# Optimization experiments

Measured on AMD Instinct MI355X. Metric: run time of the kernel, lower is better.

## Reference

```python
import jax, jax.numpy as jnp
from jax import lax
import numpy as np

D_MODEL, D_STATE, D_CONV, EXPAND = 192, 16, 3, 2
D_INNER = EXPAND * D_MODEL
B_, H_, W_ = 8, 128, 128
PAD = (D_CONV - 1) // 2
EPS = 1e-5


def setup_inputs() -> dict:
    key = jax.random.key(0)
    ks = jax.random.split(key, 8)
    s = 0.02
    return {
        "x": jax.random.normal(ks[0], (B_, D_MODEL, H_, W_), jnp.float32),
        "w_in": jax.random.normal(ks[1], (D_MODEL, 2 * D_INNER), jnp.float32) * s,
        "w_conv": jax.random.normal(ks[2], (D_INNER, 1, D_CONV, D_CONV), jnp.float32) * s,
        "b_conv": jnp.zeros((D_INNER,), jnp.float32),
        "w_x": jax.random.normal(ks[3], (D_INNER, 2 * D_STATE), jnp.float32) * s,
        "w_dt": jax.random.normal(ks[4], (D_STATE, D_INNER), jnp.float32) * s,
        "b_dt": jnp.zeros((D_INNER,), jnp.float32),
        "D_skip": jnp.ones((D_INNER,), jnp.float32),
        "w_out": jax.random.normal(ks[5], (D_INNER, D_MODEL), jnp.float32) * s,
        "gamma": jnp.ones((D_INNER,), jnp.float32),
        "beta": jnp.zeros((D_INNER,), jnp.float32),
    }


def _ss2d(x, w_in, w_conv, b_conv, w_x, w_dt, b_dt, D_skip, w_out, gamma, beta):
    B, C, H, W = x.shape
    L = H * W
    # NOTE: faithful to torch: x.reshape(B, H*W, C) on an NCHW tensor is a raw
    # row-major reinterpretation (same semantics as jnp.reshape), not a transpose.
    x_flat = x.reshape(B, L, C)
    x_proj = x_flat @ w_in                     # [B, L, 2*d_inner]
    x_inner, z = jnp.split(x_proj, 2, axis=-1)
    # depthwise conv over spatial dims
    xc = jnp.transpose(x_inner, (0, 2, 1)).reshape(B, D_INNER, H, W)
    xc = lax.conv_general_dilated(
        xc, w_conv, window_strides=(1, 1), padding=[(PAD, PAD), (PAD, PAD)],
        dimension_numbers=("NCHW", "OIHW", "NCHW"), feature_group_count=D_INNER,
    ) + b_conv[None, :, None, None]
    xc = jax.nn.silu(xc)
    xc = jnp.transpose(xc.reshape(B, D_INNER, L), (0, 2, 1))   # [B, L, d_inner]
    x_ssm = xc @ w_x                                            # [B, L, 2*d_state]
    B_ssm, C_ssm = jnp.split(x_ssm, 2, axis=-1)
    dt = jax.nn.softplus(B_ssm @ w_dt + b_dt)                   # [B, L, d_inner]
    # Original: deltaB = dt[...,None]*B_ssm[:,:,None,:]; einsum('blid,bld->bli', deltaB, C_ssm)
    # == dt * sum_d(B_ssm*C_ssm)  (deltaA is computed but never used -> dropped)
    bc = jnp.sum(B_ssm * C_ssm, axis=-1, keepdims=True)         # [B, L, 1]
    y = dt * bc + xc * D_skip                                   # [B, L, d_inner]
    y = y * jax.nn.silu(z)
    mu = jnp.mean(y, axis=-1, keepdims=True)
    var = jnp.mean(jnp.square(y - mu), axis=-1, keepdims=True)
    y = (y - mu) * lax.rsqrt(var + EPS) * gamma + beta
    out = y @ w_out                                             # [B, L, d_model]
    return jnp.transpose(out, (0, 2, 1)).reshape(B, C, H, W)


def reference(x, w_in, w_conv, b_conv, w_x, w_dt, b_dt, D_skip, w_out, gamma, beta):
    return _ss2d(x, w_in, w_conv, b_conv, w_x, w_dt, b_dt, D_skip, w_out, gamma, beta)
```

## Files before the change

### kernel.cpp

```cpp
#include <hip/hip_runtime.h>
#include <hip/hip_bf16.h>

typedef __bf16 bf16x8 __attribute__((ext_vector_type(8)));
typedef __bf16 bf16x4 __attribute__((ext_vector_type(4)));
typedef float  f32x4  __attribute__((ext_vector_type(4)));

__device__ __forceinline__ f32x4 mfma16(bf16x8 a, bf16x8 b, f32x4 c) {
    return __builtin_amdgcn_mfma_f32_16x16x32_bf16(a, b, c, 0, 0, 0);
}
__device__ __forceinline__ float silu_f(float v) { return v / (1.f + __expf(-v)); }
__device__ __forceinline__ float softplus_fast(float v) {
    float r = __logf(1.f + __expf(v));
    return v > 15.f ? v : r;
}

#define CC 192
#define DI 384
#define LL 16384
#define HH 128
#define WW 128

__global__ void k0_prep(const float* __restrict__ w_in, const float* __restrict__ w_x,
                        const float* __restrict__ w_dt, const float* __restrict__ w_out,
                        __bf16* __restrict__ wt_in, __bf16* __restrict__ wt_x,
                        __bf16* __restrict__ wt_dt, __bf16* __restrict__ wt_out) {
    int tid = blockIdx.x * blockDim.x + threadIdx.x;
    int nth = gridDim.x * blockDim.x;
    for (int i = tid; i < 768 * 192; i += nth) { int n = i / 192, k = i % 192; wt_in[i] = (__bf16)w_in[k * 768 + n]; }
    for (int i = tid; i < 32 * 384;  i += nth) { int n = i / 384, k = i % 384; wt_x[i]  = (__bf16)w_x[k * 32 + n]; }
    for (int i = tid; i < 384 * 16;  i += nth) { int ch = i / 16, k = i % 16;  wt_dt[i] = (__bf16)w_dt[k * 384 + ch]; }
    for (int i = tid; i < 192 * 384; i += nth) { int n = i / 384, k = i % 384; wt_out[i] = (__bf16)w_out[k * 192 + n]; }
}

__global__ __launch_bounds__(256, 4) void k1_proj(
        const float* __restrict__ x, const __bf16* __restrict__ wt_in,
        __bf16* __restrict__ xin, __bf16* __restrict__ zsb) {
    __shared__ __attribute__((aligned(16))) __bf16 wb[4 * 2 * 32 * 68];
    const int tid = threadIdx.x;
    const int lane = tid & 63, wv = tid >> 6;
    const int lq = lane & 15, quad = lane >> 4;
    const long mbase = (long)blockIdx.x * 128;
    __bf16* wbase = wb + wv * (2 * 32 * 68);

    bf16x8 af[2][6];
#pragma unroll
    for (int mt = 0; mt < 2; mt++) {
        const float* xr = x + (mbase + wv * 32 + mt * 16 + lq) * CC;
#pragma unroll
        for (int ks = 0; ks < 6; ks++) {
            float4 v0 = *(const float4*)(xr + ks * 32 + quad * 8);
            float4 v1 = *(const float4*)(xr + ks * 32 + quad * 8 + 4);
            bf16x8 t;
            t[0] = (__bf16)v0.x; t[1] = (__bf16)v0.y; t[2] = (__bf16)v0.z; t[3] = (__bf16)v0.w;
            t[4] = (__bf16)v1.x; t[5] = (__bf16)v1.y; t[6] = (__bf16)v1.z; t[7] = (__bf16)v1.w;
            af[mt][ks] = t;
        }
    }

    for (int nc = 0; nc < 12; nc++) {
        f32x4 A0[4], A1[4];
#pragma unroll
        for (int nt = 0; nt < 4; nt++) {
            A0[nt] = (f32x4){0.f, 0.f, 0.f, 0.f};
            A1[nt] = (f32x4){0.f, 0.f, 0.f, 0.f};
#pragma unroll
            for (int ks = 0; ks < 6; ks++) {
                bf16x8 bf = *(const bf16x8*)(wt_in + (long)(nc * 64 + nt * 16 + lq) * CC + ks * 32 + quad * 8);
                A0[nt] = mfma16(af[0][ks], bf, A0[nt]);
                A1[nt] = mfma16(af[1][ks], bf, A1[nt]);
            }
        }
        const bool isz = (nc >= 6);
        __bf16* bb = wbase + (nc & 1) * (32 * 68);
#pragma unroll
        for (int nt = 0; nt < 4; nt++) {
#pragma unroll
            for (int r = 0; r < 4; r++) {
                float v0 = A0[nt][r], v1 = A1[nt][r];
                if (isz) { v0 = silu_f(v0); v1 = silu_f(v1); }
                bb[(quad * 4 + r) * 68 + nt * 16 + lq] = (__bf16)v0;
                bb[(16 + quad * 4 + r) * 68 + nt * 16 + lq] = (__bf16)v1;
            }
        }
        __builtin_amdgcn_wave_barrier();
        __bf16* dst = isz ? zsb : xin;
        const int chb = (isz ? nc - 6 : nc) * 64;
#pragma unroll
        for (int k = 0; k < 4; k++) {
            int u = lane + k * 64;
            int row = u >> 3, c8 = u & 7;
            unsigned long long lo = *(const unsigned long long*)(&bb[row * 68 + c8 * 8]);
            unsigned long long hi = *(const unsigned long long*)(&bb[row * 68 + c8 * 8 + 4]);
            ulonglong2 val; val.x = lo; val.y = hi;
            *(ulonglong2*)(dst + (mbase + wv * 32 + row) * DI + chb + c8 * 8) = val;
        }
        __builtin_amdgcn_wave_barrier();
    }
}

__global__ __launch_bounds__(512, 4) void k3_ssm(
        const __bf16* __restrict__ xin, const __bf16* __restrict__ zsb,
        const __bf16* __restrict__ wtx, const __bf16* __restrict__ wtdt,
        const __bf16* __restrict__ wtout, const float* __restrict__ wconv,
        const float* __restrict__ bconv, const float* __restrict__ bdt,
        const float* __restrict__ dskip, const float* __restrict__ gamma,
        const float* __restrict__ beta, float* __restrict__ out) {
    __shared__ __attribute__((aligned(16))) float smem0[13056];
    __shared__ __attribute__((aligned(16))) __bf16 dts[64 * 200];
    __shared__ float bcarr[64];
    __bf16* xcb = (__bf16*)smem0;
    float* otile = smem0;

    const int tid = threadIdx.x;
    const int lane = tid & 63, wv = tid >> 6;
    const int lq = lane & 15, quad = lane >> 4;
    const int t0g = blockIdx.x * 64;

    const int te = tid >> 3, part = tid & 7;
    const long tok = t0g + te;

    bf16x8 zpre[6];
#pragma unroll
    for (int h = 0; h < 2; h++)
#pragma unroll
        for (int g = 0; g < 3; g++)
            zpre[h * 3 + g] = *(const bf16x8*)(zsb + tok * DI + h * 192 + part * 24 + g * 8);

    float* wcvs = (float*)dts;
    float* bcvs = wcvs + 9 * 384;
    for (int u = tid; u < 9 * 384; u += 512) { int ch = u / 9, tap = u % 9; wcvs[tap * 384 + ch] = wconv[u]; }
    for (int u = tid; u < 384; u += 512) bcvs[u] = bconv[u];
    __syncthreads();

    const int hblk = (t0g & (LL - 1)) >> 7;
    const int w0 = t0g & 127;
#pragma unroll
    for (int k = 0; k < 6; k++) {
        int u = tid + k * 512;
        int t = u / 48, c8 = u % 48;
        long tk = t0g + t;
        float acc[8];
        float4 b0 = *(const float4*)(bcvs + c8 * 8);
        float4 b1 = *(const float4*)(bcvs + c8 * 8 + 4);
        acc[0] = b0.x; acc[1] = b0.y; acc[2] = b0.z; acc[3] = b0.w;
        acc[4] = b1.x; acc[5] = b1.y; acc[6] = b1.z; acc[7] = b1.w;
#pragma unroll
        for (int dy = -1; dy <= 1; dy++) {
            int h2 = hblk + dy;
            if (h2 < 0 || h2 >= HH) continue;
#pragma unroll
            for (int dx = -1; dx <= 1; dx++) {
                int w2 = w0 + t + dx;
                if (w2 < 0 || w2 >= WW) continue;
                bf16x8 v = *(const bf16x8*)(xin + (tk + dy * WW + dx) * (long)DI + c8 * 8);
                const float* wp = &wcvs[((dy + 1) * 3 + (dx + 1)) * 384 + c8 * 8];
#pragma unroll
                for (int j = 0; j < 8; j++) acc[j] += (float)v[j] * wp[j];
            }
        }
        bf16x8 r;
#pragma unroll
        for (int j = 0; j < 8; j++) r[j] = (__bf16)silu_f(acc[j]);
        *(bf16x8*)(&xcb[t * 392 + c8 * 8]) = r;
    }
    __syncthreads();

    float* Bf = (float*)dts;
    float* Cf = Bf + 64 * 20;
    {
        const int wt = wv & 3, wsel = wv >> 2;
        f32x4 a4 = {0.f, 0.f, 0.f, 0.f};
#pragma unroll
        for (int ks = 0; ks < 12; ks++) {
            bf16x8 a = *(const bf16x8*)(&xcb[(wt * 16 + lq) * 392 + ks * 32 + quad * 8]);
            bf16x8 b = *(const bf16x8*)(wtx + (wsel * 16 + lq) * 384 + ks * 32 + quad * 8);
            a4 = mfma16(a, b, a4);
        }
        float* dstf = wsel ? Cf : Bf;
#pragma unroll
        for (int r = 0; r < 4; r++)
            dstf[(wt * 16 + quad * 4 + r) * 20 + lq] = a4[r];
    }
    __syncthreads();

    {
        int t = tid >> 3;
        int s0 = (tid & 7) * 2;
        float p = Bf[t * 20 + s0] * Cf[t * 20 + s0] + Bf[t * 20 + s0 + 1] * Cf[t * 20 + s0 + 1];
        p += __shfl_xor(p, 1, 64);
        p += __shfl_xor(p, 2, 64);
        p += __shfl_xor(p, 4, 64);
        if ((lane & 7) == 0) bcarr[t] = p;
    }
    bf16x8 zero8;
#pragma unroll
    for (int j = 0; j < 8; j++) zero8[j] = (__bf16)0.f;
    bf16x8 aA[4];
#pragma unroll
    for (int mt = 0; mt < 4; mt++) {
        if (quad < 2) {
            const float* bp = Bf + (mt * 16 + lq) * 20 + quad * 8;
            f32x4 lo = *(const f32x4*)(bp);
            f32x4 hi = *(const f32x4*)(bp + 4);
            bf16x8 t8;
            t8[0] = (__bf16)lo[0]; t8[1] = (__bf16)lo[1]; t8[2] = (__bf16)lo[2]; t8[3] = (__bf16)lo[3];
            t8[4] = (__bf16)hi[0]; t8[5] = (__bf16)hi[1]; t8[6] = (__bf16)hi[2]; t8[7] = (__bf16)hi[3];
            aA[mt] = t8;
        } else {
            aA[mt] = zero8;
        }
    }
    __syncthreads();

    float s1 = 0.f, s2 = 0.f;

#pragma unroll
    for (int h = 0; h < 2; h++) {
        f32x4 dacc[2][4];
        float bdtv[2];
#pragma unroll
        for (int j = 0; j < 2; j++) {
            const int tile = wv + 8 * j;
            if (tile < 12) {
                int chg = h * 192 + tile * 16 + lq;
                bf16x8 bf = (quad < 2) ? *(const bf16x8*)(wtdt + (long)chg * 16 + quad * 8) : zero8;
                bdtv[j] = bdt[chg];
#pragma unroll
                for (int mt = 0; mt < 4; mt++) {
                    f32x4 z4 = {0.f, 0.f, 0.f, 0.f};
                    dacc[j][mt] = mfma16(aA[mt], bf, z4);
                }
            }
        }
#pragma unroll
        for (int j = 0; j < 2; j++) {
            const int tile = wv + 8 * j;
            if (tile < 12) {
#pragma unroll
                for (int mt = 0; mt < 4; mt++)
#pragma unroll
                    for (int r = 0; r < 4; r++)
                        dts[(mt * 16 + quad * 4 + r) * 200 + tile * 16 + lq] =
                            (__bf16)(dacc[j][mt][r] + bdtv[j]);
            }
        }
        __syncthreads();

#pragma unroll
        for (int g = 0; g < 3; g++) {
            const int chl = part * 24 + g * 8;
            const int chg = h * 192 + chl;
            bf16x8 d8 = *(const bf16x8*)(&dts[te * 200 + chl]);
            bf16x8 xc8 = *(const bf16x8*)(&xcb[te * 392 + chg]);
            bf16x8 z8 = zpre[h * 3 + g];
            float4 d0 = *(const float4*)(dskip + chg);
            float4 d1 = *(const float4*)(dskip + chg + 4);
            float ds[8] = {d0.x, d0.y, d0.z, d0.w, d1.x, d1.y, d1.z, d1.w};
            const float bcv = bcarr[te];
#pragma unroll
            for (int j = 0; j < 8; j++) {
                float dtv = softplus_fast((float)d8[j]);
                float yv = (dtv * bcv + (float)xc8[j] * ds[j]) * (float)z8[j];
                s1 += yv; s2 += yv * yv;
                xc8[j] = (__bf16)yv;
            }
            *(bf16x8*)(&xcb[te * 392 + chg]) = xc8;
        }
        __syncthreads();
    }

    {
        s1 += __shfl_xor(s1, 1, 64); s2 += __shfl_xor(s2, 1, 64);
        s1 += __shfl_xor(s1, 2, 64); s2 += __shfl_xor(s2, 2, 64);
        s1 += __shfl_xor(s1, 4, 64); s2 += __shfl_xor(s2, 4, 64);
        float mu = s1 * (1.f / 384.f);
        float var = s2 * (1.f / 384.f) - mu * mu;
        float rstd = rsqrtf(var + 1e-5f);
#pragma unroll
        for (int gg = 0; gg < 6; gg++) {
            const int h2 = gg / 3, g3 = gg % 3;
            const int ch = h2 * 192 + part * 24 + g3 * 8;
            bf16x8 v = *(const bf16x8*)(&xcb[te * 392 + ch]);
            float4 g0 = *(const float4*)(gamma + ch);
            float4 g1 = *(const float4*)(gamma + ch + 4);
            float4 be0 = *(const float4*)(beta + ch);
            float4 be1 = *(const float4*)(beta + ch + 4);
            float gm[8] = {g0.x, g0.y, g0.z, g0.w, g1.x, g1.y, g1.z, g1.w};
            float bt[8] = {be0.x, be0.y, be0.z, be0.w, be1.x, be1.y, be1.z, be1.w};
#pragma unroll
            for (int j = 0; j < 8; j++) v[j] = (__bf16)(((float)v[j] - mu) * rstd * gm[j] + bt[j]);
            *(bf16x8*)(&xcb[te * 392 + ch]) = v;
        }
    }
    __syncthreads();

    {
        const int mh = wv >> 2, nb = (wv & 3) * 3;
        f32x4 acc[3][2];
#pragma unroll
        for (int j = 0; j < 3; j++)
#pragma unroll
            for (int m2 = 0; m2 < 2; m2++) acc[j][m2] = (f32x4){0.f, 0.f, 0.f, 0.f};
#pragma unroll
        for (int ks = 0; ks < 12; ks++) {
            bf16x8 bfr[3];
#pragma unroll
            for (int j = 0; j < 3; j++) {
                int c = (nb + j) * 16 + lq;
                bfr[j] = *(const bf16x8*)(wtout + (long)c * 384 + ks * 32 + quad * 8);
            }
#pragma unroll
            for (int m2 = 0; m2 < 2; m2++) {
                bf16x8 afr = *(const bf16x8*)(&xcb[((mh * 2 + m2) * 16 + lq) * 392 + ks * 32 + quad * 8]);
#pragma unroll
                for (int j = 0; j < 3; j++) acc[j][m2] = mfma16(afr, bfr[j], acc[j][m2]);
            }
        }
        __syncthreads();
#pragma unroll
        for (int j = 0; j < 3; j++) {
            int c = (nb + j) * 16 + lq;
#pragma unroll
            for (int m2 = 0; m2 < 2; m2++)
#pragma unroll
                for (int r = 0; r < 4; r++)
                    otile[c * 68 + (mh * 2 + m2) * 16 + quad * 4 + r] = acc[j][m2][r];
        }
    }
    __syncthreads();

    {
        const int bimg = t0g >> 14;
        const int l0 = t0g & (LL - 1);
#pragma unroll
        for (int k = 0; k < 6; k++) {
            int u = tid + k * 512;
            int c = u >> 4, j = u & 15;
            float4 v = *(const float4*)(&otile[c * 68 + j * 4]);
            *(float4*)(out + ((long)(bimg * CC + c)) * LL + l0 + j * 4) = v;
        }
    }
}

extern "C" void kernel_launch(void* const* d_in, const int* in_sizes, int n_in,
                              void* d_out, int out_size, void* d_ws, size_t ws_size,
                              hipStream_t stream) {
    (void)in_sizes; (void)n_in; (void)out_size; (void)ws_size;
    const float* x      = (const float*)d_in[0];
    const float* w_in   = (const float*)d_in[1];
    const float* w_conv = (const float*)d_in[2];
    const float* b_conv = (const float*)d_in[3];
    const float* w_x    = (const float*)d_in[4];
    const float* w_dt   = (const float*)d_in[5];
    const float* b_dt   = (const float*)d_in[6];
    const float* D_skip = (const float*)d_in[7];
    const float* w_out  = (const float*)d_in[8];
    const float* gamma  = (const float*)d_in[9];
    const float* beta   = (const float*)d_in[10];
    float* out = (float*)d_out;

    char* ws = (char*)d_ws;
    __bf16* wt_in  = (__bf16*)(ws);
    __bf16* wt_x   = (__bf16*)(ws + 294912);
    __bf16* wt_dt  = (__bf16*)(ws + 319488);
    __bf16* wt_out = (__bf16*)(ws + 331776);
    __bf16* xin    = (__bf16*)(ws + 479232);
    __bf16* zsb    = (__bf16*)(ws + 479232 + 100663296);

    k0_prep<<<96, 256, 0, stream>>>(w_in, w_x, w_dt, w_out, wt_in, wt_x, wt_dt, wt_out);
    k1_proj<<<1024, 256, 0, stream>>>(x, wt_in, xin, zsb);
    k3_ssm<<<2048, 512, 0, stream>>>(xin, zsb, wt_x, wt_dt, wt_out, w_conv, b_conv,
                                     b_dt, D_skip, gamma, beta, out);
}
```

Baseline: 561.2 us.

## Stage swizzled w_in tiles into LDS with double-buffered async loads in projection kernel

The input-projection kernel used to read weight fragments straight from global memory for every MFMA. It now pre-swizzles w_in into 64-column chunks in the prep kernel and stages each chunk into a double-buffered LDS array with global_load_lds, prefetching the next chunk while computing the current one. The XOR swizzle is meant to avoid LDS bank conflicts on the fragment reads. The cost is a block-wide barrier per chunk, more shared memory, and lower occupancy hints (launch bounds drop to 2 on both k1 and k3).

```diff
diff --git a/kernel.cpp b/kernel.cpp
--- a/kernel.cpp
+++ b/kernel.cpp
@@ -26,21 +26,27 @@
                         __bf16* __restrict__ wt_dt, __bf16* __restrict__ wt_out) {
     int tid = blockIdx.x * blockDim.x + threadIdx.x;
     int nth = gridDim.x * blockDim.x;
-    for (int i = tid; i < 768 * 192; i += nth) { int n = i / 192, k = i % 192; wt_in[i] = (__bf16)w_in[k * 768 + n]; }
+    for (int i = tid; i < 768 * 192; i += nth) {
+        int nf = i / 192, k = i % 192;
+        int nc = nf >> 6, n = nf & 63;
+        int e = (n * 192 + k) ^ ((n & 7) << 3);
+        wt_in[nc * 12288 + e] = (__bf16)w_in[k * 768 + nf];
+    }
     for (int i = tid; i < 32 * 384;  i += nth) { int n = i / 384, k = i % 384; wt_x[i]  = (__bf16)w_x[k * 32 + n]; }
     for (int i = tid; i < 384 * 16;  i += nth) { int ch = i / 16, k = i % 16;  wt_dt[i] = (__bf16)w_dt[k * 384 + ch]; }
     for (int i = tid; i < 192 * 384; i += nth) { int n = i / 384, k = i % 384; wt_out[i] = (__bf16)w_out[k * 192 + n]; }
 }
 
-__global__ __launch_bounds__(256, 4) void k1_proj(
+__global__ __launch_bounds__(256, 2) void k1_proj(
         const float* __restrict__ x, const __bf16* __restrict__ wt_in,
         __bf16* __restrict__ xin, __bf16* __restrict__ zsb) {
-    __shared__ __attribute__((aligned(16))) __bf16 wb[4 * 2 * 32 * 68];
+    __shared__ __attribute__((aligned(16))) __bf16 Bs[2][12288];
+    __shared__ __attribute__((aligned(16))) __bf16 bounce[4][32 * 68];
     const int tid = threadIdx.x;
     const int lane = tid & 63, wv = tid >> 6;
     const int lq = lane & 15, quad = lane >> 4;
     const long mbase = (long)blockIdx.x * 128;
-    __bf16* wbase = wb + wv * (2 * 32 * 68);
+    __bf16* bb = &bounce[wv][0];
 
     bf16x8 af[2][6];
 #pragma unroll
@@ -57,7 +63,26 @@
         }
     }
 
+    auto stage = [&](int b, int nc) {
+        const char* src = (const char*)(wt_in + nc * 12288);
+        char* dst = (char*)&Bs[b][0];
+#pragma unroll
+        for (int i = 0; i < 6; i++) {
+            int off = (wv * 6 + i) * 1024;
+            __builtin_amdgcn_global_load_lds(
+                (const __attribute__((address_space(1))) void*)(src + off + lane * 16),
+                (__attribute__((address_space(3))) void*)(dst + off),
+                16, 0, 0);
+        }
+    };
+
+    stage(0, 0);
+    __syncthreads();
+
+    int buf = 0;
     for (int nc = 0; nc < 12; nc++) {
+        if (nc < 11) stage(buf ^ 1, nc + 1);
+
         f32x4 A0[4], A1[4];
 #pragma unroll
         for (int nt = 0; nt < 4; nt++) {
@@ -65,13 +90,14 @@
             A1[nt] = (f32x4){0.f, 0.f, 0.f, 0.f};
 #pragma unroll
             for (int ks = 0; ks < 6; ks++) {
-                bf16x8 bf = *(const bf16x8*)(wt_in + (long)(nc * 64 + nt * 16 + lq) * CC + ks * 32 + quad * 8);
+                const int row = nt * 16 + lq;
+                const int e = (row * 192 + ks * 32 + quad * 8) ^ ((lq & 7) << 3);
+                bf16x8 bf = *(const bf16x8*)(&Bs[buf][e]);
                 A0[nt] = mfma16(af[0][ks], bf, A0[nt]);
                 A1[nt] = mfma16(af[1][ks], bf, A1[nt]);
             }
         }
         const bool isz = (nc >= 6);
-        __bf16* bb = wbase + (nc & 1) * (32 * 68);
 #pragma unroll
         for (int nt = 0; nt < 4; nt++) {
 #pragma unroll
@@ -94,11 +120,12 @@
             ulonglong2 val; val.x = lo; val.y = hi;
             *(ulonglong2*)(dst + (mbase + wv * 32 + row) * DI + chb + c8 * 8) = val;
         }
-        __builtin_amdgcn_wave_barrier();
-    }
-}
-
-__global__ __launch_bounds__(512, 4) void k3_ssm(
+        __syncthreads();
+        buf ^= 1;
+    }
+}
+
+__global__ __launch_bounds__(512, 2) void k3_ssm(
         const __bf16* __restrict__ xin, const __bf16* __restrict__ zsb,
         const __bf16* __restrict__ wtx, const __bf16* __restrict__ wtdt,
         const __bf16* __restrict__ wtout, const float* __restrict__ wconv,
```

Measured after the change: 550.3 us. About the same (-2.0%).
